# Kernel optimization log

Measured on AMD Instinct MI355X. Metric: run time of the kernel, lower is better.

Reference implementation:

```python
import jax, jax.numpy as jnp
import numpy as np


def setup_inputs() -> dict:
    key = jax.random.key(0)
    k1, k2 = jax.random.split(key)
    x = jax.random.normal(k1, (8, 2048, 512), dtype=jnp.float32)
    kernel = jax.random.normal(k2, (3, 512, 64), dtype=jnp.float32) * 0.02
    return {"x": x, "kernel": kernel}


def reference(x, kernel):
    # x: [B, S, D], kernel: [3, D, H]
    wq = jnp.einsum('bsd,dh->bsh', x, kernel[0])
    wk = jnp.einsum('bsd,dh->bsh', x, kernel[1])
    wv = jnp.einsum('bsd,dh->bsh', x, kernel[2])
    # scores: [B, S, S]; original uses hard-coded 1/sqrt(64) scale
    scores = jnp.einsum('bqh,bkh->bqk', wq, wk) / jnp.asarray(64.0 ** 0.5, dtype=x.dtype)
    attn = jax.nn.softmax(scores, axis=-1)
    return jnp.einsum('bqk,bkh->bqh', attn, wv)
```

## Files before the change

kernel.cpp:

```cpp
#include <hip/hip_runtime.h>
#include <hip/hip_bf16.h>
#include <stdint.h>

typedef short s8v  __attribute__((ext_vector_type(8)));
typedef float f4v  __attribute__((ext_vector_type(4)));
typedef float f16v __attribute__((ext_vector_type(16)));

static __device__ __forceinline__ uint16_t f2bf(float f) {
    union { float f; uint32_t u; } v; v.f = f;
    uint32_t r = v.u + 0x7fffu + ((v.u >> 16) & 1u);
    return (uint16_t)(r >> 16);
}
static __device__ __forceinline__ uint32_t pk2(float lo, float hi) {
    return ((uint32_t)f2bf(hi) << 16) | (uint32_t)f2bf(lo);
}
static __device__ __forceinline__ int swz(int row, int col) {
    return row * 64 + (col ^ ((row & 7) * 8));
}

__global__ __launch_bounds__(256) void wtrans(const float* __restrict__ w,
                                              uint16_t* __restrict__ wt) {
    __shared__ uint16_t lds[64][72];
    const int tid = threadIdx.x;
    const int p = blockIdx.x >> 3;
    const int kb = (blockIdx.x & 7) * 64;
    const float scale = (p == 0) ? 0.18033688011112042f : 1.0f;

    #pragma unroll
    for (int i = 0; i < 16; ++i) {
        const int idx = i * 256 + tid;
        const int k = idx >> 6, h = idx & 63;
        lds[h][k] = f2bf(w[((size_t)(p * 512) + kb + k) * 64 + h] * scale);
    }
    __syncthreads();
    #pragma unroll
    for (int j = 0; j < 2; ++j) {
        const int c = j * 256 + tid;
        const int h = c >> 3, kc = (c & 7) * 8;
        *(s8v*)(wt + (size_t)(p * 64 + h) * 512 + kb + kc) = *(const s8v*)&lds[h][kc];
    }
}

__global__ __launch_bounds__(512) void qkv_proj(const float* __restrict__ x,
                                                const uint16_t* __restrict__ wt,
                                                uint16_t* __restrict__ qo,
                                                uint16_t* __restrict__ ko,
                                                uint16_t* __restrict__ vto) {
    __shared__ uint16_t xs[2][64][72];
    __shared__ uint16_t wsh[2][96][72];

    const int tid  = threadIdx.x;
    const int lane = tid & 63;
    const int wv   = tid >> 6;
    const int rowg = wv >> 1;
    const int colg = wv & 1;
    const int row0 = (blockIdx.x >> 1) * 64;
    const int c0   = (blockIdx.x & 1) * 96;
    const int lr = lane & 15;
    const int lg = lane >> 4;

    f4v acc[3];
    #pragma unroll
    for (int i = 0; i < 3; ++i) acc[i] = (f4v){0.f, 0.f, 0.f, 0.f};

    const int srow = tid >> 3;
    const int scol = (tid & 7) * 8;

    {
        const float* xp = x + (size_t)(row0 + srow) * 512 + scol;
        float4 a = *(const float4*)xp, bq = *(const float4*)(xp + 4);
        s8v xv;
        xv[0] = (short)f2bf(a.x);  xv[1] = (short)f2bf(a.y);
        xv[2] = (short)f2bf(a.z);  xv[3] = (short)f2bf(a.w);
        xv[4] = (short)f2bf(bq.x); xv[5] = (short)f2bf(bq.y);
        xv[6] = (short)f2bf(bq.z); xv[7] = (short)f2bf(bq.w);
        *(s8v*)&xs[0][srow][scol] = xv;
        *(s8v*)&wsh[0][srow][scol] = *(const s8v*)(wt + (size_t)(c0 + srow) * 512 + scol);
        if (tid < 256)
            *(s8v*)&wsh[0][64 + srow][scol] = *(const s8v*)(wt + (size_t)(c0 + 64 + srow) * 512 + scol);
    }
    __syncthreads();

    int buf = 0;
    for (int kb = 0; kb < 512; kb += 64) {
        const bool more = (kb + 64 < 512);
        float4 xa, xb; s8v w0r, w1r;
        if (more) {
            const float* xp = x + (size_t)(row0 + srow) * 512 + kb + 64 + scol;
            xa = *(const float4*)xp;
            xb = *(const float4*)(xp + 4);
            w0r = *(const s8v*)(wt + (size_t)(c0 + srow) * 512 + kb + 64 + scol);
            if (tid < 256)
                w1r = *(const s8v*)(wt + (size_t)(c0 + 64 + srow) * 512 + kb + 64 + scol);
        }
        s8v a0 = *(const s8v*)&xs[buf][rowg * 16 + lr][lg * 8];
        s8v a1 = *(const s8v*)&xs[buf][rowg * 16 + lr][32 + lg * 8];
        #pragma unroll
        for (int ct = 0; ct < 3; ++ct) {
            const int wr = colg * 48 + ct * 16 + lr;
            s8v b0 = *(const s8v*)&wsh[buf][wr][lg * 8];
            s8v b1 = *(const s8v*)&wsh[buf][wr][32 + lg * 8];
            acc[ct] = __builtin_amdgcn_mfma_f32_16x16x32_bf16(a0, b0, acc[ct], 0, 0, 0);
            acc[ct] = __builtin_amdgcn_mfma_f32_16x16x32_bf16(a1, b1, acc[ct], 0, 0, 0);
        }
        if (more) {
            s8v xv;
            xv[0] = (short)f2bf(xa.x); xv[1] = (short)f2bf(xa.y);
            xv[2] = (short)f2bf(xa.z); xv[3] = (short)f2bf(xa.w);
            xv[4] = (short)f2bf(xb.x); xv[5] = (short)f2bf(xb.y);
            xv[6] = (short)f2bf(xb.z); xv[7] = (short)f2bf(xb.w);
            *(s8v*)&xs[buf ^ 1][srow][scol] = xv;
            *(s8v*)&wsh[buf ^ 1][srow][scol] = w0r;
            if (tid < 256) *(s8v*)&wsh[buf ^ 1][64 + srow][scol] = w1r;
        }
        __syncthreads();
        buf ^= 1;
    }

    #pragma unroll
    for (int ct = 0; ct < 3; ++ct) {
        const int c = c0 + colg * 48 + ct * 16 + lr;
        const int p = c >> 6, h = c & 63;
        #pragma unroll
        for (int r = 0; r < 4; ++r) {
            const int row = row0 + rowg * 16 + lg * 4 + r;
            const uint16_t val = f2bf(acc[ct][r]);
            if (p == 0)      qo[(size_t)row * 64 + h] = val;
            else if (p == 1) ko[(size_t)row * 64 + h] = val;
            else {
                const int bb = row >> 11, s = row & 2047;
                vto[((size_t)bb * 64 + h) * 2048 + s] = val;
            }
        }
    }
}

__global__ __launch_bounds__(256) void attn(const uint16_t* __restrict__ q,
                                            const uint16_t* __restrict__ k,
                                            const uint16_t* __restrict__ vt,
                                            float* __restrict__ opart,
                                            float* __restrict__ lpart,
                                            float* __restrict__ out,
                                            int nsplit) {
    __shared__ uint16_t kls[2][4096];
    __shared__ uint16_t vls[2][4096];

    const int tid = threadIdx.x;
    const int l   = tid & 63;
    const int wv  = tid >> 6;
    const int hi  = l >> 5;
    const int lo  = l & 31;
    const int sp   = blockIdx.x % nsplit;
    const int bq   = blockIdx.x / nsplit;
    const int b    = bq >> 4;
    const int qblk = bq & 15;
    const int kspan = 2048 / nsplit;
    const int k0 = sp * kspan;
    const int ntiles = kspan / 64;
    const int qb0 = qblk * 128 + wv * 32;

    const uint16_t* qb = q  + (size_t)b * 2048 * 64;
    const uint16_t* kp = k  + (size_t)b * 2048 * 64;
    const uint16_t* vb = vt + (size_t)b * 64 * 2048;

    s8v qf[4];
    #pragma unroll
    for (int d = 0; d < 4; ++d)
        qf[d] = *(const s8v*)(qb + (size_t)(qb0 + lo) * 64 + d * 16 + hi * 8);

    f16v O0, O1;
    #pragma unroll
    for (int i = 0; i < 16; ++i) { O0[i] = 0.f; O1[i] = 0.f; }
    float lsum = 0.f;

    const int r1 = tid >> 3,         cc1 = (tid & 7) * 8;
    const int r2 = (tid + 256) >> 3, cc2 = (tid & 7) * 8;

    *(s8v*)&kls[0][swz(r1, cc1)] = *(const s8v*)(kp + (size_t)(k0 + r1) * 64 + cc1);
    *(s8v*)&kls[0][swz(r2, cc2)] = *(const s8v*)(kp + (size_t)(k0 + r2) * 64 + cc2);
    *(s8v*)&vls[0][swz(r1, cc1)] = *(const s8v*)(vb + (size_t)r1 * 2048 + k0 + cc1);
    *(s8v*)&vls[0][swz(r2, cc2)] = *(const s8v*)(vb + (size_t)r2 * 2048 + k0 + cc2);
    __syncthreads();

    int buf = 0;
    for (int t = 0; t < ntiles; ++t) {
        const int kb2 = k0 + t * 64;
        const bool more = (t + 1 < ntiles);
        s8v sk1, sk2, sv1, sv2;
        if (more) {
            sk1 = *(const s8v*)(kp + (size_t)(kb2 + 64 + r1) * 64 + cc1);
            sk2 = *(const s8v*)(kp + (size_t)(kb2 + 64 + r2) * 64 + cc2);
            sv1 = *(const s8v*)(vb + (size_t)r1 * 2048 + kb2 + 64 + cc1);
            sv2 = *(const s8v*)(vb + (size_t)r2 * 2048 + kb2 + 64 + cc2);
        }

        #pragma unroll
        for (int s = 0; s < 2; ++s) {
            f16v sacc;
            #pragma unroll
            for (int i = 0; i < 16; ++i) sacc[i] = 0.f;
            #pragma unroll
            for (int d = 0; d < 4; ++d) {
                s8v kf = *(const s8v*)&kls[buf][swz(s * 32 + lo, d * 16 + hi * 8)];
                sacc = __builtin_amdgcn_mfma_f32_32x32x16_bf16(kf, qf[d], sacc, 0, 0, 0);
            }
            float p[16];
            #pragma unroll
            for (int r = 0; r < 16; ++r) p[r] = exp2f(sacc[r]);
            #pragma unroll
            for (int r = 0; r < 16; ++r) lsum += p[r];
            uint32_t w[8];
            #pragma unroll
            for (int j = 0; j < 8; ++j) w[j] = pk2(p[2 * j], p[2 * j + 1]);
            #pragma unroll
            for (int m = 0; m < 2; ++m) {
                const uint32_t s0 = hi ? w[4 * m + 0] : w[4 * m + 2];
                const uint32_t s1 = hi ? w[4 * m + 1] : w[4 * m + 3];
                const uint32_t r0 = (uint32_t)__shfl_xor((int)s0, 32, 64);
                const uint32_t rr = (uint32_t)__shfl_xor((int)s1, 32, 64);
                union { uint32_t u[4]; s8v v; } af;
                af.u[0] = hi ? r0 : w[4 * m + 0];
                af.u[1] = hi ? rr : w[4 * m + 1];
                af.u[2] = hi ? w[4 * m + 2] : r0;
                af.u[3] = hi ? w[4 * m + 3] : rr;
                const int g = s * 2 + m;
                s8v vf0 = *(const s8v*)&vls[buf][swz(lo,      g * 16 + hi * 8)];
                s8v vf1 = *(const s8v*)&vls[buf][swz(32 + lo, g * 16 + hi * 8)];
                O0 = __builtin_amdgcn_mfma_f32_32x32x16_bf16(af.v, vf0, O0, 0, 0, 0);
                O1 = __builtin_amdgcn_mfma_f32_32x32x16_bf16(af.v, vf1, O1, 0, 0, 0);
            }
        }

        if (more) {
            *(s8v*)&kls[buf ^ 1][swz(r1, cc1)] = sk1;
            *(s8v*)&kls[buf ^ 1][swz(r2, cc2)] = sk2;
            *(s8v*)&vls[buf ^ 1][swz(r1, cc1)] = sv1;
            *(s8v*)&vls[buf ^ 1][swz(r2, cc2)] = sv2;
        }
        __syncthreads();
        buf ^= 1;
    }

    lsum += __shfl_xor(lsum, 32, 64);

    if (nsplit == 1) {
        const float inv = 1.0f / lsum;
        #pragma unroll
        for (int r = 0; r < 16; ++r) {
            const int qrow = (r & 3) + 8 * (r >> 2) + 4 * hi;
            const size_t grow = (size_t)b * 2048 + qb0 + qrow;
            out[grow * 64 + lo]      = O0[r] * inv;
            out[grow * 64 + 32 + lo] = O1[r] * inv;
        }
    } else {
        #pragma unroll
        for (int r = 0; r < 16; ++r) {
            const int qrow = (r & 3) + 8 * (r >> 2) + 4 * hi;
            const size_t grow = (size_t)sp * 16384 + (size_t)b * 2048 + qb0 + qrow;
            opart[grow * 64 + lo]      = O0[r];
            opart[grow * 64 + 32 + lo] = O1[r];
        }
        if (l < 32)
            lpart[(size_t)sp * 16384 + (size_t)b * 2048 + qb0 + l] = lsum;
    }
}

__global__ __launch_bounds__(256) void combine(const float* __restrict__ opart,
                                               const float* __restrict__ lpart,
                                               float* __restrict__ out) {
    const int idx = blockIdx.x * 256 + threadIdx.x;
    const int row = idx >> 4;
    const int hq = (idx & 15) * 4;

    const float inv = 1.0f / (lpart[row] + lpart[16384 + row] +
                              lpart[2 * 16384 + row] + lpart[3 * 16384 + row]);

    const float4 o0 = *(const float4*)(opart + ((size_t)0 * 16384 + row) * 64 + hq);
    const float4 o1 = *(const float4*)(opart + ((size_t)1 * 16384 + row) * 64 + hq);
    const float4 o2 = *(const float4*)(opart + ((size_t)2 * 16384 + row) * 64 + hq);
    const float4 o3 = *(const float4*)(opart + ((size_t)3 * 16384 + row) * 64 + hq);

    float4 res;
    res.x = (o0.x + o1.x + o2.x + o3.x) * inv;
    res.y = (o0.y + o1.y + o2.y + o3.y) * inv;
    res.z = (o0.z + o1.z + o2.z + o3.z) * inv;
    res.w = (o0.w + o1.w + o2.w + o3.w) * inv;
    *(float4*)(out + (size_t)row * 64 + hq) = res;
}

extern "C" void kernel_launch(void* const* d_in, const int* in_sizes, int n_in,
                              void* d_out, int out_size, void* d_ws, size_t ws_size,
                              hipStream_t stream) {
    const float* x = (const float*)d_in[0];
    const float* w = (const float*)d_in[1];
    char* ws = (char*)d_ws;
    uint16_t* qw = (uint16_t*)(ws);
    uint16_t* kw = (uint16_t*)(ws + 2097152);
    uint16_t* vw = (uint16_t*)(ws + 4194304);
    uint16_t* wt = (uint16_t*)(ws + 6291456);
    float*  opart = (float*)(ws + 6488064);
    float*  lpart = (float*)(ws + 23265280);
    float* out = (float*)d_out;

    const int nsplit = (ws_size >= 23527424) ? 4 : 1;

    wtrans<<<24, 256, 0, stream>>>(w, wt);
    qkv_proj<<<512, 512, 0, stream>>>(x, wt, qw, kw, vw);
    attn<<<128 * nsplit, 256, 0, stream>>>(qw, kw, vw, opart, lpart, out, nsplit);
    if (nsplit > 1) combine<<<1024, 256, 0, stream>>>(opart, lpart, out);
}
```

Before: 112.0 us.

## Split x bf16 conversion into its own kernel and stage GEMM tiles via global_load_lds

Adds a standalone xconv kernel that converts x to bf16 in workspace. The QKV projection is rewritten as qkv_gemm, which uses 128x96 tiles and 256-thread blocks with a 2x6 accumulator grid per wave, and loads tiles straight from global memory into LDS with global_load_lds. The aim is to take the conversion and register staging out of the GEMM inner loop and reuse each B fragment across more MFMAs. The cost is an extra launch and an extra write and read of a 16MB bf16 copy of x. The unswizzled LDS layout may cause bank conflicts, and the larger workspace threshold can silently drop attention to nsplit=1.

```diff
diff --git a/kernel.cpp b/kernel.cpp
--- a/kernel.cpp
+++ b/kernel.cpp
@@ -16,6 +16,11 @@
 }
 static __device__ __forceinline__ int swz(int row, int col) {
     return row * 64 + (col ^ ((row & 7) * 8));
+}
+static __device__ __forceinline__ void gload_lds16(const void* g, void* l) {
+    __builtin_amdgcn_global_load_lds(
+        (const __attribute__((address_space(1))) uint32_t*)g,
+        (__attribute__((address_space(3))) uint32_t*)l, 16, 0, 0);
 }
 
 __global__ __launch_bounds__(256) void wtrans(const float* __restrict__ w,
@@ -41,95 +46,91 @@
     }
 }
 
-__global__ __launch_bounds__(512) void qkv_proj(const float* __restrict__ x,
+__global__ __launch_bounds__(256) void xconv(const float* __restrict__ x,
+                                             uint16_t* __restrict__ xb) {
+    const int i = (blockIdx.x * 256 + threadIdx.x) * 8;
+    const float4 a = *(const float4*)(x + i);
+    const float4 b = *(const float4*)(x + i + 4);
+    s8v v;
+    v[0] = (short)f2bf(a.x); v[1] = (short)f2bf(a.y);
+    v[2] = (short)f2bf(a.z); v[3] = (short)f2bf(a.w);
+    v[4] = (short)f2bf(b.x); v[5] = (short)f2bf(b.y);
+    v[6] = (short)f2bf(b.z); v[7] = (short)f2bf(b.w);
+    *(s8v*)(xb + i) = v;
+}
+
+__global__ __launch_bounds__(256) void qkv_gemm(const uint16_t* __restrict__ xb,
                                                 const uint16_t* __restrict__ wt,
                                                 uint16_t* __restrict__ qo,
                                                 uint16_t* __restrict__ ko,
                                                 uint16_t* __restrict__ vto) {
-    __shared__ uint16_t xs[2][64][72];
-    __shared__ uint16_t wsh[2][96][72];
+    __shared__ __align__(16) uint16_t As[2][128 * 64];
+    __shared__ __align__(16) uint16_t Bs[2][96 * 64];
 
     const int tid  = threadIdx.x;
     const int lane = tid & 63;
-    const int wv   = tid >> 6;
-    const int rowg = wv >> 1;
-    const int colg = wv & 1;
-    const int row0 = (blockIdx.x >> 1) * 64;
+    const int wid  = tid >> 6;
+    const int row0 = (blockIdx.x >> 1) * 128;
     const int c0   = (blockIdx.x & 1) * 96;
     const int lr = lane & 15;
     const int lg = lane >> 4;
-
-    f4v acc[3];
-    #pragma unroll
-    for (int i = 0; i < 3; ++i) acc[i] = (f4v){0.f, 0.f, 0.f, 0.f};
-
-    const int srow = tid >> 3;
-    const int scol = (tid & 7) * 8;
-
-    {
-        const float* xp = x + (size_t)(row0 + srow) * 512 + scol;
-        float4 a = *(const float4*)xp, bq = *(const float4*)(xp + 4);
-        s8v xv;
-        xv[0] = (short)f2bf(a.x);  xv[1] = (short)f2bf(a.y);
-        xv[2] = (short)f2bf(a.z);  xv[3] = (short)f2bf(a.w);
-        xv[4] = (short)f2bf(bq.x); xv[5] = (short)f2bf(bq.y);
-        xv[6] = (short)f2bf(bq.z); xv[7] = (short)f2bf(bq.w);
-        *(s8v*)&xs[0][srow][scol] = xv;
-        *(s8v*)&wsh[0][srow][scol] = *(const s8v*)(wt + (size_t)(c0 + srow) * 512 + scol);
-        if (tid < 256)
-            *(s8v*)&wsh[0][64 + srow][scol] = *(const s8v*)(wt + (size_t)(c0 + 64 + srow) * 512 + scol);
-    }
+    const int gr = tid >> 3;
+    const int gc = (tid & 7) * 8;
+
+    f4v acc[2][6];
+    #pragma unroll
+    for (int i = 0; i < 2; ++i)
+        #pragma unroll
+        for (int j = 0; j < 6; ++j) acc[i][j] = (f4v){0.f, 0.f, 0.f, 0.f};
+
+    auto STAGE = [&](int bf, int kb) {
+        #pragma unroll
+        for (int i = 0; i < 4; ++i)
+            gload_lds16(xb + (size_t)(row0 + i * 32 + gr) * 512 + kb + gc,
+                        &As[bf][i * 2048 + wid * 512]);
+        #pragma unroll
+        for (int i = 0; i < 3; ++i)
+            gload_lds16(wt + (size_t)(c0 + i * 32 + gr) * 512 + kb + gc,
+                        &Bs[bf][i * 2048 + wid * 512]);
+    };
+
+    STAGE(0, 0);
     __syncthreads();
 
     int buf = 0;
-    for (int kb = 0; kb < 512; kb += 64) {
-        const bool more = (kb + 64 < 512);
-        float4 xa, xb; s8v w0r, w1r;
-        if (more) {
-            const float* xp = x + (size_t)(row0 + srow) * 512 + kb + 64 + scol;
-            xa = *(const float4*)xp;
-            xb = *(const float4*)(xp + 4);
-            w0r = *(const s8v*)(wt + (size_t)(c0 + srow) * 512 + kb + 64 + scol);
-            if (tid < 256)
-                w1r = *(const s8v*)(wt + (size_t)(c0 + 64 + srow) * 512 + kb + 64 + scol);
-        }
-        s8v a0 = *(const s8v*)&xs[buf][rowg * 16 + lr][lg * 8];
-        s8v a1 = *(const s8v*)&xs[buf][rowg * 16 + lr][32 + lg * 8];
-        #pragma unroll
-        for (int ct = 0; ct < 3; ++ct) {
-            const int wr = colg * 48 + ct * 16 + lr;
-            s8v b0 = *(const s8v*)&wsh[buf][wr][lg * 8];
-            s8v b1 = *(const s8v*)&wsh[buf][wr][32 + lg * 8];
-            acc[ct] = __builtin_amdgcn_mfma_f32_16x16x32_bf16(a0, b0, acc[ct], 0, 0, 0);
-            acc[ct] = __builtin_amdgcn_mfma_f32_16x16x32_bf16(a1, b1, acc[ct], 0, 0, 0);
-        }
-        if (more) {
-            s8v xv;
-            xv[0] = (short)f2bf(xa.x); xv[1] = (short)f2bf(xa.y);
-            xv[2] = (short)f2bf(xa.z); xv[3] = (short)f2bf(xa.w);
-            xv[4] = (short)f2bf(xb.x); xv[5] = (short)f2bf(xb.y);
-            xv[6] = (short)f2bf(xb.z); xv[7] = (short)f2bf(xb.w);
-            *(s8v*)&xs[buf ^ 1][srow][scol] = xv;
-            *(s8v*)&wsh[buf ^ 1][srow][scol] = w0r;
-            if (tid < 256) *(s8v*)&wsh[buf ^ 1][64 + srow][scol] = w1r;
+    for (int t = 0; t < 8; ++t) {
+        if (t < 7) STAGE(buf ^ 1, (t + 1) * 64);
+        #pragma unroll
+        for (int kk = 0; kk < 2; ++kk) {
+            s8v a0 = *(const s8v*)&As[buf][(wid * 32 + lr) * 64 + kk * 32 + lg * 8];
+            s8v a1 = *(const s8v*)&As[buf][(wid * 32 + 16 + lr) * 64 + kk * 32 + lg * 8];
+            #pragma unroll
+            for (int ct = 0; ct < 6; ++ct) {
+                s8v b = *(const s8v*)&Bs[buf][(ct * 16 + lr) * 64 + kk * 32 + lg * 8];
+                acc[0][ct] = __builtin_amdgcn_mfma_f32_16x16x32_bf16(a0, b, acc[0][ct], 0, 0, 0);
+                acc[1][ct] = __builtin_amdgcn_mfma_f32_16x16x32_bf16(a1, b, acc[1][ct], 0, 0, 0);
+            }
         }
         __syncthreads();
         buf ^= 1;
     }
 
     #pragma unroll
-    for (int ct = 0; ct < 3; ++ct) {
-        const int c = c0 + colg * 48 + ct * 16 + lr;
-        const int p = c >> 6, h = c & 63;
-        #pragma unroll
-        for (int r = 0; r < 4; ++r) {
-            const int row = row0 + rowg * 16 + lg * 4 + r;
-            const uint16_t val = f2bf(acc[ct][r]);
-            if (p == 0)      qo[(size_t)row * 64 + h] = val;
-            else if (p == 1) ko[(size_t)row * 64 + h] = val;
-            else {
-                const int bb = row >> 11, s = row & 2047;
-                vto[((size_t)bb * 64 + h) * 2048 + s] = val;
+    for (int rt = 0; rt < 2; ++rt) {
+        #pragma unroll
+        for (int ct = 0; ct < 6; ++ct) {
+            const int c = c0 + ct * 16 + lr;
+            const int p = c >> 6, h = c & 63;
+            #pragma unroll
+            for (int r = 0; r < 4; ++r) {
+                const int row = row0 + wid * 32 + rt * 16 + lg * 4 + r;
+                const uint16_t val = f2bf(acc[rt][ct][r]);
+                if (p == 0)      qo[(size_t)row * 64 + h] = val;
+                else if (p == 1) ko[(size_t)row * 64 + h] = val;
+                else {
+                    const int bb = row >> 11, s = row & 2047;
+                    vto[((size_t)bb * 64 + h) * 2048 + s] = val;
+                }
             }
         }
     }
@@ -298,14 +299,16 @@
     uint16_t* kw = (uint16_t*)(ws + 2097152);
     uint16_t* vw = (uint16_t*)(ws + 4194304);
     uint16_t* wt = (uint16_t*)(ws + 6291456);
-    float*  opart = (float*)(ws + 6488064);
-    float*  lpart = (float*)(ws + 23265280);
+    uint16_t* xb = (uint16_t*)(ws + 6488064);
+    float*  opart = (float*)(ws + 23265280);
+    float*  lpart = (float*)(ws + 40042496);
     float* out = (float*)d_out;
 
-    const int nsplit = (ws_size >= 23527424) ? 4 : 1;
+    const int nsplit = (ws_size >= 40304640) ? 4 : 1;
 
     wtrans<<<24, 256, 0, stream>>>(w, wt);
-    qkv_proj<<<512, 512, 0, stream>>>(x, wt, qw, kw, vw);
+    xconv<<<4096, 256, 0, stream>>>(x, xb);
+    qkv_gemm<<<256, 256, 0, stream>>>(xb, wt, qw, kw, vw);
     attn<<<128 * nsplit, 256, 0, stream>>>(qw, kw, vw, opart, lpart, out, nsplit);
     if (nsplit > 1) combine<<<1024, 256, 0, stream>>>(opart, lpart, out);
 }
```

Result: slower. 120.6 us (+7.6%).
